# Kernel optimization log

Measured on AMD Instinct MI355X. Metric: run time of the kernel, lower is better.

The kernel has to match this reference:

```python
import jax, jax.numpy as jnp
import numpy as np

L, Q, H, B = 200, 21, 128, 256
LQ = L * Q


def _dca_mask():
    # Faithful to the original code: loop bounds use l_alphabet (q), not seq_len.
    m = np.zeros((LQ, LQ), np.float32)
    for i in range(Q):
        for j in range(i):
            m[i * Q:(i + 1) * Q, j * Q:(j + 1) * Q] = 1.0
    return jnp.asarray(m)


def _row_mask():
    # row_mask[l, d] = 1 if d < (l+1)*q : valid prefix rows for FFNet i=l+1
    return jnp.asarray((np.arange(LQ)[None, :] < (np.arange(1, L) * Q)[:, None]).astype(np.float32))


def setup_inputs() -> dict:
    key = jax.random.key(0)
    ks = jax.random.split(key, 12)
    # one-hot encoded sequences (B, L, Q)
    idx = jax.random.randint(ks[0], (B, L), 0, Q)
    x = jax.nn.one_hot(idx, Q, dtype=jnp.float32)
    row_mask = _row_mask()  # (L-1, LQ)
    W1 = 0.02 * jax.random.normal(ks[1], (L - 1, LQ, H), dtype=jnp.float32) * row_mask[:, :, None]
    return {
        "x": x,
        "DCA_bias": jnp.zeros((LQ,), jnp.float32),
        "DCA_weights": 0.01 * jax.random.normal(ks[2], (LQ, LQ), dtype=jnp.float32),
        "w0": 0.1 * jax.random.normal(ks[3], (Q,), dtype=jnp.float32),   # nn_bias0 weight (q,1) collapsed
        "b0": 0.1 * jax.random.normal(ks[4], (Q,), dtype=jnp.float32),
        "W1": W1,
        "b1": 0.02 * jax.random.normal(ks[5], (L - 1, H), dtype=jnp.float32),
        "W2": 0.08 * jax.random.normal(ks[6], (L - 1, H, H), dtype=jnp.float32),
        "b2": 0.02 * jax.random.normal(ks[7], (L - 1, H), dtype=jnp.float32),
        "Wout": 0.08 * jax.random.normal(ks[8], (L - 1, H, Q), dtype=jnp.float32),
        "bout": 0.02 * jax.random.normal(ks[9], (L - 1, Q), dtype=jnp.float32),
    }


def _lrelu(v):
    return jnp.where(v >= 0, v, 0.1 * v)  # negative_slope=0.1


def reference(x, DCA_bias, DCA_weights, w0, b0, W1, b1, W2, b2, Wout, bout):
    x_flat = x.reshape(x.shape[0], LQ)
    # arDCA: masked dense matmul
    logits_dca = (DCA_bias + x_flat @ (DCA_weights * _dca_mask())).reshape(-1, L, Q)
    # arNN position 0: Linear(1, q) applied to ones -> w0 + b0 broadcast over batch
    out0 = jnp.broadcast_to(w0 + b0, (x.shape[0], Q))
    # positions 1..L-1: ragged FFNets batched as padded stacked GEMMs.
    # Padded weight rows are masked to zero so x_flat @ W1_eff[l] == prefix_l @ W1_l.
    W1_eff = W1 * _row_mask()[:, :, None]          # (L-1, LQ, H)
    h1 = _lrelu(jnp.einsum('bd,ldh->blh', x_flat, W1_eff) + b1)   # (B, L-1, H)
    h2 = _lrelu(jnp.einsum('blh,lhk->blk', h1, W2) + b2)          # (B, L-1, H)
    out_rest = jnp.einsum('blh,lhq->blq', h2, Wout) + bout        # (B, L-1, Q)
    logits_nn = jnp.concatenate([out0[:, None, :], out_rest], axis=1)
    return logits_dca + logits_nn
```

## Files before the change

### kernel.cpp

```cpp
#include <hip/hip_runtime.h>


#define Lc   200
#define Qc   21
#define Hc   128
#define Bc   256
#define LQc  4200
#define LM1c 199
#define CH   48
#define NCH  5

__device__ __forceinline__ unsigned int bf16rne(float f) {
    unsigned int u = __float_as_uint(f);
    return u + 0x7fffu + ((u >> 16) & 1u);
}

__global__ __launch_bounds__(256) void k_idx(const float* __restrict__ x,
                                             unsigned char* __restrict__ idxT) {
    const int l = blockIdx.x;
    const int b = threadIdx.x;
    const float* p = x + ((size_t)b * Lc + l) * Qc;
    int id = 0;
#pragma unroll
    for (int c = 0; c < Qc; ++c) id = (p[c] > 0.5f) ? c : id;
    idxT[l * Bc + b] = (unsigned char)id;
}

__global__ __launch_bounds__(512) void k_dca(const float* __restrict__ DW,
                                             const float* __restrict__ bias,
                                             const float* __restrict__ w0,
                                             const float* __restrict__ b0,
                                             const unsigned char* __restrict__ idxT,
                                             float* __restrict__ out) {
    const int b = blockIdx.x;
    const int t = threadIdx.x;
    __shared__ int sidx[20];
    if (t < 20) sidx[t] = idxT[(t + 1) * Bc + b];
    __syncthreads();
    if (t >= 441) return;
    const int pos = t / 21, q = t - pos * 21;
    const int j = t;
    float acc = 0.f;
    for (int lr = pos + 1; lr <= 20; ++lr)
        acc += DW[(size_t)(lr * Qc + sidx[lr - 1]) * LQc + j];
    float* op = out + (size_t)b * LQc;
    if (pos == 0) op[j] = acc + bias[j] + w0[q] + b0[q];
    else          op[j] += acc;
}

__global__ __launch_bounds__(1024, 2) void k_h1(const float* __restrict__ W1,
                                                const unsigned char* __restrict__ idxT,
                                                unsigned int* __restrict__ part) {
    const int bid = blockIdx.x;
    const int l = 198 - bid / NCH, c = bid % NCH;
    const int lo = c * CH;
    if (lo > l) return;
    const int hi = (l < lo + CH - 1) ? l : lo + CH - 1;
    const int n = hi - lo + 1;

    const int t = threadIdx.x;
    const int hq = t & 31;
    const int bg = t >> 5;

    __shared__ __align__(16) float tile[2][Qc * 132];
    __shared__ __align__(16) unsigned char idxs8[CH * Bc];

    {
        const int4* isrc = (const int4*)(idxT + lo * Bc);
        int4* idst = (int4*)idxs8;
        if (t < n * 16) idst[t] = isrc[t];
    }

    const float* Wsrc = W1 + (size_t)l * (LQc * Hc) + (size_t)lo * (Qc * Hc);
    if (t < 672) {
        const float4 q = ((const float4*)Wsrc)[t];
        *(float4*)&tile[0][(t >> 5) * 132 + (t & 31) * 4] = q;
    }
    __syncthreads();

    float4 acc[8];
#pragma unroll
    for (int j = 0; j < 8; ++j) acc[j] = (float4){0.f, 0.f, 0.f, 0.f};

    int cur = 0;
    for (int k = 0; k < n; ++k) {
        float4 p;
        const bool st = (k + 1 < n) && (t < 672);
        if (st) p = ((const float4*)(Wsrc + (size_t)(k + 1) * (Qc * Hc)))[t];
        const unsigned int* ibw = (const unsigned int*)&idxs8[k * Bc + bg * 8];
        const unsigned int u0 = ibw[0], u1 = ibw[1];
        const float* tb = &tile[cur][hq * 4];
#define ACC(j, u, sh) { \
        const float4 v = *(const float4*)(tb + (int)((u >> sh) & 0xffu) * 132); \
        acc[j].x += v.x; acc[j].y += v.y; acc[j].z += v.z; acc[j].w += v.w; }
        ACC(0, u0, 0) ACC(1, u0, 8) ACC(2, u0, 16) ACC(3, u0, 24)
        ACC(4, u1, 0) ACC(5, u1, 8) ACC(6, u1, 16) ACC(7, u1, 24)
#undef ACC
        if (st) *(float4*)&tile[cur ^ 1][(t >> 5) * 132 + (t & 31) * 4] = p;
        __syncthreads();
        cur ^= 1;
    }

    unsigned int* pb = part + ((size_t)(l * NCH + c) * Bc + bg * 8) * (Hc / 2) + hq * 2;
#pragma unroll
    for (int j = 0; j < 8; ++j) {
        const unsigned int d0 = (bf16rne(acc[j].x) >> 16) | (bf16rne(acc[j].y) & 0xffff0000u);
        const unsigned int d1 = (bf16rne(acc[j].z) >> 16) | (bf16rne(acc[j].w) & 0xffff0000u);
        *(uint2*)(pb + (size_t)j * (Hc / 2)) = make_uint2(d0, d1);
    }
}

__global__ __launch_bounds__(512, 4) void k_h2(const unsigned int* __restrict__ part,
                                               const float* __restrict__ W2,
                                               const float* __restrict__ b1,
                                               const float* __restrict__ b2,
                                               const float* __restrict__ Wout,
                                               const float* __restrict__ bout,
                                               const float* __restrict__ bias,
                                               float* __restrict__ out) {
    const int d = blockIdx.x;
    const int g = d >> 4, r = d & 7, half = (d >> 3) & 1;
    const int l = g * 8 + r;
    if (l >= LM1c) return;
    const int bbase = half * 128;
    const int t = threadIdx.x;
    const int tx = t & 15, ty = t >> 4;
    __shared__ float As[16][132];
    __shared__ float Bs[16][Hc];
    __shared__ float Ts[32][132];
    __shared__ float wl[Hc][24];
    __shared__ float blsh[24];
    float acc[4][8];
#pragma unroll
    for (int i = 0; i < 4; ++i)
#pragma unroll
        for (int j = 0; j < 8; ++j) acc[i][j] = 0.f;
    {
        const float* wsrc = Wout + (size_t)l * Hc * Qc;
        for (int i = t; i < Hc * Qc; i += 512) wl[i / Qc][i % Qc] = wsrc[i];
        if (t < Hc) { wl[t][21] = 0.f; wl[t][22] = 0.f; wl[t][23] = 0.f; }
        if (t < Qc) blsh[t] = bout[l * Qc + t] + bias[(l + 1) * Qc + t];
        else if (t < 24) blsh[t] = 0.f;
    }
    const int skk = t >> 5, sms = (t & 31) * 4;
    const int am = t >> 2, akq = (t & 3) * 4;
    const int nch = l / CH + 1;
    const unsigned int* pl = part + ((size_t)(l * NCH) * Bc + bbase + am) * (Hc / 2);
    const float* W2l = W2 + (size_t)l * Hc * Hc;
    for (int ks = 0; ks < 8; ++ks) {
        const int kcu = ks * 8 + (t & 3) * 2;
        float4 a0 = {0.f, 0.f, 0.f, 0.f};
        for (int cc = 0; cc < nch; ++cc) {
            const uint2 w = *(const uint2*)(pl + (size_t)cc * Bc * (Hc / 2) + kcu);
            a0.x += __uint_as_float(w.x << 16);
            a0.y += __uint_as_float(w.x & 0xffff0000u);
            a0.z += __uint_as_float(w.y << 16);
            a0.w += __uint_as_float(w.y & 0xffff0000u);
        }
        const float4 bb = *(const float4*)(b1 + l * Hc + ks * 16 + akq);
        a0.x += bb.x; a0.y += bb.y; a0.z += bb.z; a0.w += bb.w;
        a0.x = (a0.x >= 0.f) ? a0.x : 0.1f * a0.x;
        a0.y = (a0.y >= 0.f) ? a0.y : 0.1f * a0.y;
        a0.z = (a0.z >= 0.f) ? a0.z : 0.1f * a0.z;
        a0.w = (a0.w >= 0.f) ? a0.w : 0.1f * a0.w;
        const int kb = ks * 16 + skk;
        *(float4*)&Bs[skk][sms] = *(const float4*)(W2l + (size_t)kb * Hc + sms);
        As[akq + 0][am] = a0.x; As[akq + 1][am] = a0.y;
        As[akq + 2][am] = a0.z; As[akq + 3][am] = a0.w;
        __syncthreads();
#pragma unroll
        for (int k = 0; k < 16; ++k) {
            float avr[4], bvr[8];
            *(float4*)&avr[0] = *(const float4*)&As[k][ty * 4];
            *(float4*)&bvr[0] = *(const float4*)&Bs[k][tx * 8];
            *(float4*)&bvr[4] = *(const float4*)&Bs[k][tx * 8 + 4];
#pragma unroll
            for (int i = 0; i < 4; ++i)
#pragma unroll
                for (int j = 0; j < 8; ++j) acc[i][j] += avr[i] * bvr[j];
        }
        __syncthreads();
    }
    float bz[8];
    *(float4*)&bz[0] = *(const float4*)(b2 + l * Hc + tx * 8);
    *(float4*)&bz[4] = *(const float4*)(b2 + l * Hc + tx * 8 + 4);
    float res[4][8];
#pragma unroll
    for (int i = 0; i < 4; ++i)
#pragma unroll
        for (int j = 0; j < 8; ++j) {
            float v = acc[i][j] + bz[j];
            res[i][j] = (v >= 0.f) ? v : 0.1f * v;
        }
    const int m = t & 127, qh = t >> 7;
    const int q0 = qh * 6;
    float racc[6];
#pragma unroll
    for (int qi = 0; qi < 6; ++qi) racc[qi] = 0.f;
    for (int c = 0; c < 4; ++c) {
        if ((tx >> 2) == c) {
#pragma unroll
            for (int i = 0; i < 4; ++i)
#pragma unroll
                for (int j = 0; j < 8; ++j) Ts[(tx & 3) * 8 + j][ty * 4 + i] = res[i][j];
        }
        __syncthreads();
#pragma unroll 4
        for (int rr = 0; rr < 32; ++rr) {
            const float v = Ts[rr][m];
            const float* wr = &wl[c * 32 + rr][q0];
#pragma unroll
            for (int qi = 0; qi < 6; ++qi) racc[qi] += v * wr[qi];
        }
        __syncthreads();
    }
    const int b = bbase + m;
    float* op = out + ((size_t)b * Lc + (l + 1)) * Qc;
#pragma unroll
    for (int qi = 0; qi < 6; ++qi) {
        const int qq = q0 + qi;
        if (qq < Qc) op[qq] = racc[qi] + blsh[qq];
    }
}

extern "C" void kernel_launch(void* const* d_in, const int* in_sizes, int n_in,
                              void* d_out, int out_size, void* d_ws, size_t ws_size,
                              hipStream_t stream) {
    const float* x    = (const float*)d_in[0];
    const float* bias = (const float*)d_in[1];
    const float* DW   = (const float*)d_in[2];
    const float* w0   = (const float*)d_in[3];
    const float* b0   = (const float*)d_in[4];
    const float* W1   = (const float*)d_in[5];
    const float* b1   = (const float*)d_in[6];
    const float* W2   = (const float*)d_in[7];
    const float* b2   = (const float*)d_in[8];
    const float* Wout = (const float*)d_in[9];
    const float* bout = (const float*)d_in[10];
    float* out = (float*)d_out;

    unsigned char* idxT = (unsigned char*)d_ws;
    unsigned int*  part = (unsigned int*)((char*)d_ws + 204800);

    k_idx<<<Lc, 256, 0, stream>>>(x, idxT);
    k_h1<<<LM1c * NCH, 1024, 0, stream>>>(W1, idxT, part);
    k_h2<<<400, 512, 0, stream>>>(part, W2, b1, b2, Wout, bout, bias, out);
    k_dca<<<Bc, 512, 0, stream>>>(DW, bias, w0, b0, idxT, out);
}
```

Measured before the change: 156.7 us.

## Compute h1 gather-sum with bf16 MFMA on one-hot A tiles

The h1 stage was a per-thread gather-and-add of W1 rows selected by one-hot indices. It now builds one-hot bf16 A fragments in registers and multiplies them against bf16-packed W1 tiles with 16x16x32 MFMA, two positions at a time with double-buffered LDS and register prefetch. The partial-sum layout becomes transposed (h-major), and k_h2 reads it accordingly. This trades cheap LDS gathers for matrix-core work that includes many zero multiplies, and W1 is rounded to bf16 before accumulation, which costs precision.

```diff
diff --git a/kernel.cpp b/kernel.cpp
--- a/kernel.cpp
+++ b/kernel.cpp
@@ -9,10 +9,17 @@
 #define LM1c 199
 #define CH   48
 #define NCH  5
+#define BTW  20
+
+typedef short bf16v8 __attribute__((ext_vector_type(8)));
+typedef float f32x4 __attribute__((ext_vector_type(4)));
 
 __device__ __forceinline__ unsigned int bf16rne(float f) {
     unsigned int u = __float_as_uint(f);
     return u + 0x7fffu + ((u >> 16) & 1u);
+}
+__device__ __forceinline__ unsigned int pack2(float a, float b) {
+    return (bf16rne(a) >> 16) | (bf16rne(b) & 0xffff0000u);
 }
 
 __global__ __launch_bounds__(256) void k_idx(const float* __restrict__ x,
@@ -48,9 +55,9 @@
     else          op[j] += acc;
 }
 
-__global__ __launch_bounds__(1024, 2) void k_h1(const float* __restrict__ W1,
-                                                const unsigned char* __restrict__ idxT,
-                                                unsigned int* __restrict__ part) {
+__global__ __launch_bounds__(512, 4) void k_h1(const float* __restrict__ W1,
+                                               const unsigned char* __restrict__ idxT,
+                                               unsigned int* __restrict__ partT) {
     const int bid = blockIdx.x;
     const int l = 198 - bid / NCH, c = bid % NCH;
     const int lo = c * CH;
@@ -59,58 +66,123 @@
     const int n = hi - lo + 1;
 
     const int t = threadIdx.x;
-    const int hq = t & 31;
-    const int bg = t >> 5;
-
-    __shared__ __align__(16) float tile[2][Qc * 132];
-    __shared__ __align__(16) unsigned char idxs8[CH * Bc];
+    const int lane = t & 63, w = t >> 6;
+    const int wm = w >> 1, wn = w & 1;
+    const int l15 = lane & 15;
+    const int kb = (lane >> 4) * 8;
+
+    __shared__ unsigned int Bt[2][2][128 * BTW];
 
     {
-        const int4* isrc = (const int4*)(idxT + lo * Bc);
-        int4* idst = (int4*)idxs8;
-        if (t < n * 16) idst[t] = isrc[t];
+        unsigned int* btf = &Bt[0][0][0];
+        for (int i = t; i < 2 * 2 * 128 * 9; i += 512)
+            btf[(i / 9) * BTW + 11 + (i % 9)] = 0u;
     }
 
     const float* Wsrc = W1 + (size_t)l * (LQc * Hc) + (size_t)lo * (Qc * Hc);
-    if (t < 672) {
-        const float4 q = ((const float4*)Wsrc)[t];
-        *(float4*)&tile[0][(t >> 5) * 132 + (t & 31) * 4] = q;
+
+    {
+        const int np0 = (n < 2) ? n : 2;
+        const int lim = np0 * 1408;
+#pragma unroll
+        for (int s = 0; s < 6; ++s) {
+            const int idx = s * 512 + t;
+            if (idx < lim) {
+                const int pos = idx / 1408, r = idx % 1408;
+                const int kp = r >> 7, nn = r & 127;
+                const float* wp = Wsrc + (size_t)pos * (Qc * Hc) + (2 * kp) * Hc + nn;
+                const float f0 = wp[0];
+                const float f1 = (kp < 10) ? wp[Hc] : 0.f;
+                Bt[0][pos][nn * BTW + kp] = pack2(f0, f1);
+            }
+        }
     }
     __syncthreads();
 
-    float4 acc[8];
-#pragma unroll
-    for (int j = 0; j < 8; ++j) acc[j] = (float4){0.f, 0.f, 0.f, 0.f};
-
+    f32x4 acc[4][4];
+#pragma unroll
+    for (int i = 0; i < 4; ++i)
+#pragma unroll
+        for (int j = 0; j < 4; ++j) acc[i][j] = (f32x4){0.f, 0.f, 0.f, 0.f};
+
+#define MT(MTI, IV) { \
+    unsigned int a0 = (((IV) == kb + 0) ? 0x3F80u : 0u) | (((IV) == kb + 1) ? 0x3F800000u : 0u); \
+    unsigned int a1 = (((IV) == kb + 2) ? 0x3F80u : 0u) | (((IV) == kb + 3) ? 0x3F800000u : 0u); \
+    unsigned int a2 = (((IV) == kb + 4) ? 0x3F80u : 0u) | (((IV) == kb + 5) ? 0x3F800000u : 0u); \
+    unsigned int a3 = (((IV) == kb + 6) ? 0x3F80u : 0u) | (((IV) == kb + 7) ? 0x3F800000u : 0u); \
+    AU au; au.u.x = a0; au.u.y = a1; au.u.z = a2; au.u.w = a3; \
+    acc[MTI][0] = __builtin_amdgcn_mfma_f32_16x16x32_bf16(au.v, bf0, acc[MTI][0], 0, 0, 0); \
+    acc[MTI][1] = __builtin_amdgcn_mfma_f32_16x16x32_bf16(au.v, bf1, acc[MTI][1], 0, 0, 0); \
+    acc[MTI][2] = __builtin_amdgcn_mfma_f32_16x16x32_bf16(au.v, bf2, acc[MTI][2], 0, 0, 0); \
+    acc[MTI][3] = __builtin_amdgcn_mfma_f32_16x16x32_bf16(au.v, bf3, acc[MTI][3], 0, 0, 0); }
+
+    union AU { uint4 u; bf16v8 v; };
+
+    const int ngroups = (n + 1) / 2;
     int cur = 0;
-    for (int k = 0; k < n; ++k) {
-        float4 p;
-        const bool st = (k + 1 < n) && (t < 672);
-        if (st) p = ((const float4*)(Wsrc + (size_t)(k + 1) * (Qc * Hc)))[t];
-        const unsigned int* ibw = (const unsigned int*)&idxs8[k * Bc + bg * 8];
-        const unsigned int u0 = ibw[0], u1 = ibw[1];
-        const float* tb = &tile[cur][hq * 4];
-#define ACC(j, u, sh) { \
-        const float4 v = *(const float4*)(tb + (int)((u >> sh) & 0xffu) * 132); \
-        acc[j].x += v.x; acc[j].y += v.y; acc[j].z += v.z; acc[j].w += v.w; }
-        ACC(0, u0, 0) ACC(1, u0, 8) ACC(2, u0, 16) ACC(3, u0, 24)
-        ACC(4, u1, 0) ACC(5, u1, 8) ACC(6, u1, 16) ACC(7, u1, 24)
-#undef ACC
-        if (st) *(float4*)&tile[cur ^ 1][(t >> 5) * 132 + (t & 31) * 4] = p;
+    for (int g = 0; g < ngroups; ++g) {
+        float pf0[6], pf1[6];
+        bool pv[6];
+        const int bnext = (g + 1) * 2;
+        const int npn = (bnext < n) ? ((n - bnext < 2) ? n - bnext : 2) : 0;
+        const int limn = npn * 1408;
+#pragma unroll
+        for (int s = 0; s < 6; ++s) {
+            const int idx = s * 512 + t;
+            pv[s] = (idx < limn);
+            if (pv[s]) {
+                const int pos = idx / 1408, r = idx % 1408;
+                const int kp = r >> 7, nn = r & 127;
+                const float* wp = Wsrc + (size_t)(bnext + pos) * (Qc * Hc) + (2 * kp) * Hc + nn;
+                pf0[s] = wp[0];
+                pf1[s] = (kp < 10) ? wp[Hc] : 0.f;
+            }
+        }
+        const int gb = g * 2;
+#pragma unroll
+        for (int pos = 0; pos < 2; ++pos) {
+            if (gb + pos >= n) break;
+            const int lp = lo + gb + pos;
+            const unsigned char* ip = idxT + lp * Bc + wm * 64 + l15;
+            const int iv0 = ip[0], iv1 = ip[16], iv2 = ip[32], iv3 = ip[48];
+            const unsigned int* bp = &Bt[cur][pos][0];
+            const int nbase = wn * 64 + l15;
+            const bf16v8 bf0 = *(const bf16v8*)(bp + (nbase +  0) * BTW + (kb >> 1));
+            const bf16v8 bf1 = *(const bf16v8*)(bp + (nbase + 16) * BTW + (kb >> 1));
+            const bf16v8 bf2 = *(const bf16v8*)(bp + (nbase + 32) * BTW + (kb >> 1));
+            const bf16v8 bf3 = *(const bf16v8*)(bp + (nbase + 48) * BTW + (kb >> 1));
+            MT(0, iv0) MT(1, iv1) MT(2, iv2) MT(3, iv3)
+        }
+#pragma unroll
+        for (int s = 0; s < 6; ++s) {
+            if (pv[s]) {
+                const int idx = s * 512 + t;
+                const int pos = idx / 1408, r = idx % 1408;
+                const int kp = r >> 7, nn = r & 127;
+                Bt[cur ^ 1][pos][nn * BTW + kp] = pack2(pf0[s], pf1[s]);
+            }
+        }
         __syncthreads();
         cur ^= 1;
     }
-
-    unsigned int* pb = part + ((size_t)(l * NCH + c) * Bc + bg * 8) * (Hc / 2) + hq * 2;
-#pragma unroll
-    for (int j = 0; j < 8; ++j) {
-        const unsigned int d0 = (bf16rne(acc[j].x) >> 16) | (bf16rne(acc[j].y) & 0xffff0000u);
-        const unsigned int d1 = (bf16rne(acc[j].z) >> 16) | (bf16rne(acc[j].w) & 0xffff0000u);
-        *(uint2*)(pb + (size_t)j * (Hc / 2)) = make_uint2(d0, d1);
-    }
-}
-
-__global__ __launch_bounds__(512, 4) void k_h2(const unsigned int* __restrict__ part,
+#undef MT
+
+    unsigned int* pb = partT + (size_t)(l * NCH + c) * Hc * (Bc / 2);
+#pragma unroll
+    for (int mt = 0; mt < 4; ++mt)
+#pragma unroll
+        for (int nt = 0; nt < 4; ++nt) {
+            const f32x4 a = acc[mt][nt];
+            const int nn = wn * 64 + nt * 16 + l15;
+            const int m0 = wm * 64 + mt * 16 + ((lane >> 4) << 2);
+            uint2 d;
+            d.x = pack2(a[0], a[1]);
+            d.y = pack2(a[2], a[3]);
+            *(uint2*)(pb + (size_t)nn * (Bc / 2) + (m0 >> 1)) = d;
+        }
+}
+
+__global__ __launch_bounds__(512, 4) void k_h2(const unsigned int* __restrict__ partT,
                                                const float* __restrict__ W2,
                                                const float* __restrict__ b1,
                                                const float* __restrict__ b2,
@@ -143,30 +215,31 @@
         else if (t < 24) blsh[t] = 0.f;
     }
     const int skk = t >> 5, sms = (t & 31) * 4;
-    const int am = t >> 2, akq = (t & 3) * 4;
+    const int k16 = t >> 5, mq = t & 31;
     const int nch = l / CH + 1;
-    const unsigned int* pl = part + ((size_t)(l * NCH) * Bc + bbase + am) * (Hc / 2);
+    const unsigned int* plT = partT + (size_t)(l * NCH) * Hc * (Bc / 2)
+                              + (bbase >> 1) + mq * 2;
     const float* W2l = W2 + (size_t)l * Hc * Hc;
     for (int ks = 0; ks < 8; ++ks) {
-        const int kcu = ks * 8 + (t & 3) * 2;
-        float4 a0 = {0.f, 0.f, 0.f, 0.f};
+        const int h = ks * 16 + k16;
+        float s0 = 0.f, s1 = 0.f, s2 = 0.f, s3 = 0.f;
         for (int cc = 0; cc < nch; ++cc) {
-            const uint2 w = *(const uint2*)(pl + (size_t)cc * Bc * (Hc / 2) + kcu);
-            a0.x += __uint_as_float(w.x << 16);
-            a0.y += __uint_as_float(w.x & 0xffff0000u);
-            a0.z += __uint_as_float(w.y << 16);
-            a0.w += __uint_as_float(w.y & 0xffff0000u);
-        }
-        const float4 bb = *(const float4*)(b1 + l * Hc + ks * 16 + akq);
-        a0.x += bb.x; a0.y += bb.y; a0.z += bb.z; a0.w += bb.w;
-        a0.x = (a0.x >= 0.f) ? a0.x : 0.1f * a0.x;
-        a0.y = (a0.y >= 0.f) ? a0.y : 0.1f * a0.y;
-        a0.z = (a0.z >= 0.f) ? a0.z : 0.1f * a0.z;
-        a0.w = (a0.w >= 0.f) ? a0.w : 0.1f * a0.w;
-        const int kb = ks * 16 + skk;
-        *(float4*)&Bs[skk][sms] = *(const float4*)(W2l + (size_t)kb * Hc + sms);
-        As[akq + 0][am] = a0.x; As[akq + 1][am] = a0.y;
-        As[akq + 2][am] = a0.z; As[akq + 3][am] = a0.w;
+            const uint2 wv = *(const uint2*)(plT + ((size_t)cc * Hc + h) * (Bc / 2));
+            s0 += __uint_as_float(wv.x << 16);
+            s1 += __uint_as_float(wv.x & 0xffff0000u);
+            s2 += __uint_as_float(wv.y << 16);
+            s3 += __uint_as_float(wv.y & 0xffff0000u);
+        }
+        const float bb = b1[l * Hc + h];
+        s0 += bb; s1 += bb; s2 += bb; s3 += bb;
+        s0 = (s0 >= 0.f) ? s0 : 0.1f * s0;
+        s1 = (s1 >= 0.f) ? s1 : 0.1f * s1;
+        s2 = (s2 >= 0.f) ? s2 : 0.1f * s2;
+        s3 = (s3 >= 0.f) ? s3 : 0.1f * s3;
+        const int kb2 = ks * 16 + skk;
+        *(float4*)&Bs[skk][sms] = *(const float4*)(W2l + (size_t)kb2 * Hc + sms);
+        As[k16][mq * 4 + 0] = s0; As[k16][mq * 4 + 1] = s1;
+        As[k16][mq * 4 + 2] = s2; As[k16][mq * 4 + 3] = s3;
         __syncthreads();
 #pragma unroll
         for (int k = 0; k < 16; ++k) {
@@ -197,8 +270,8 @@
     float racc[6];
 #pragma unroll
     for (int qi = 0; qi < 6; ++qi) racc[qi] = 0.f;
-    for (int c = 0; c < 4; ++c) {
-        if ((tx >> 2) == c) {
+    for (int cq = 0; cq < 4; ++cq) {
+        if ((tx >> 2) == cq) {
 #pragma unroll
             for (int i = 0; i < 4; ++i)
 #pragma unroll
@@ -208,7 +281,7 @@
 #pragma unroll 4
         for (int rr = 0; rr < 32; ++rr) {
             const float v = Ts[rr][m];
-            const float* wr = &wl[c * 32 + rr][q0];
+            const float* wr = &wl[cq * 32 + rr][q0];
 #pragma unroll
             for (int qi = 0; qi < 6; ++qi) racc[qi] += v * wr[qi];
         }
@@ -240,10 +313,10 @@
     float* out = (float*)d_out;
 
     unsigned char* idxT = (unsigned char*)d_ws;
-    unsigned int*  part = (unsigned int*)((char*)d_ws + 204800);
+    unsigned int*  partT = (unsigned int*)((char*)d_ws + 204800);
 
     k_idx<<<Lc, 256, 0, stream>>>(x, idxT);
-    k_h1<<<LM1c * NCH, 1024, 0, stream>>>(W1, idxT, part);
-    k_h2<<<400, 512, 0, stream>>>(part, W2, b1, b2, Wout, bout, bias, out);
+    k_h1<<<LM1c * NCH, 512, 0, stream>>>(W1, idxT, partT);
+    k_h2<<<400, 512, 0, stream>>>(partT, W2, b1, b2, Wout, bout, bias, out);
     k_dca<<<Bc, 512, 0, stream>>>(DW, bias, w0, b0, idxT, out);
 }
```

Measured after the change: 272.5 us. 73.9% more time.
